# Performance work log

Hardware: AMD Instinct MI355X
Metric: run time of the kernel (lower is better)

## Reference

```python
import jax, jax.numpy as jnp
import numpy as np

CONF_THRES = 0.25
IOU_THRES = 0.45
MAX_DET = 1000
MAX_WH = 4096.0   # class offset for per-class NMS (yolov5 trick)
TOPK = 2048       # pre-NMS candidate cap (fixed-shape stand-in for max_nms)


def _xywh2xyxy(b):
    cx, cy, w, h = b[..., 0], b[..., 1], b[..., 2], b[..., 3]
    return jnp.stack([cx - w * 0.5, cy - h * 0.5, cx + w * 0.5, cy + h * 0.5], axis=-1)


def _box_iou(a, b):
    # a, b: [K, 4] in xyxy -> [K, K] pairwise IoU
    lt = jnp.maximum(a[:, None, :2], b[None, :, :2])
    rb = jnp.minimum(a[:, None, 2:], b[None, :, 2:])
    wh = jnp.clip(rb - lt, 0.0)
    inter = wh[..., 0] * wh[..., 1]
    area_a = (a[:, 2] - a[:, 0]) * (a[:, 3] - a[:, 1])
    area_b = (b[:, 2] - b[:, 0]) * (b[:, 3] - b[:, 1])
    return inter / (area_a[:, None] + area_b[None, :] - inter + 1e-7)


def _nms_single(pred):
    # pred: [N, 5+C] = (cx, cy, w, h, obj, cls...)
    obj = pred[:, 4]
    cls_prob = pred[:, 5:]
    cls_conf = jnp.max(cls_prob, axis=-1)
    cls_id = jnp.argmax(cls_prob, axis=-1)
    score = obj * cls_conf                      # conf = obj_conf * cls_conf (best class)
    valid = (obj > CONF_THRES) & (score > CONF_THRES)
    score = jnp.where(valid, score, 0.0)
    boxes = _xywh2xyxy(pred[:, :4])

    # keep top-K candidates by confidence (sorted descending)
    tops, idx = jax.lax.top_k(score, TOPK)
    boxes_k = boxes[idx]                        # [K, 4]
    cls_k = cls_id[idx]                         # [K]
    val_k = tops > 0.0

    # per-class NMS via class offset
    shifted = boxes_k + (cls_k.astype(boxes_k.dtype) * MAX_WH)[:, None]
    iou = _box_iou(shifted, shifted)            # [K, K]

    j = jnp.arange(TOPK)

    def body(i, keep):
        # if box i survives, suppress lower-scored boxes with IoU > thresh
        sup = keep[i] & (iou[i] > IOU_THRES) & (j > i)
        return keep & ~sup

    keep = jax.lax.fori_loop(0, TOPK, body, val_k)

    # gather up to MAX_DET kept detections (already score-sorted)
    fs, fi = jax.lax.top_k(jnp.where(keep, tops, -1.0), MAX_DET)
    ok = fs > 0.0
    det_boxes = jnp.where(ok[:, None], boxes_k[fi], 0.0)
    det_score = jnp.where(ok, tops[fi], 0.0)
    det_cls = jnp.where(ok, cls_k[fi].astype(det_boxes.dtype), -1.0)
    # [MAX_DET, 6] = (x1, y1, x2, y2, conf, cls); padded rows have conf 0, cls -1
    return jnp.concatenate([det_boxes, det_score[:, None], det_cls[:, None]], axis=-1)


def setup_inputs() -> dict:
    key = jax.random.key(0)
    raw = jax.random.uniform(key, (16, 25200, 85), dtype=jnp.float32)
    xy = raw[..., 0:2] * 640.0            # centers within a 640x640 image
    wh = raw[..., 2:4] * 120.0 + 2.0      # box sizes in [2, 122]
    rest = raw[..., 4:]                   # obj + class probs in [0, 1)
    pred = jnp.concatenate([xy, wh, rest], axis=-1)
    return {"pred": pred}


def reference(pred):
    return jax.vmap(_nms_single)(pred)
```

## Files before the change

kernel.cpp:

```cpp
#include <hip/hip_runtime.h>
#include <stdint.h>

#pragma clang fp contract(off)

#define BB 16
#define NN 25200
#define ROW 85
#define NCLS 80
#define TK 2048
#define SORTN 4096
#define NBIN 4096
#define MAXDET 1000
#define CONF 0.25f
#define IOUT 0.45f
#define SROWS 64
#define STH 0x3E800000u
#define MCAP 256

typedef float fvec4 __attribute__((ext_vector_type(4)));

#define AS1 __attribute__((address_space(1)))
#define AS3 __attribute__((address_space(3)))

__global__ __launch_bounds__(128) void score_kernel(const float* __restrict__ pred,
                                                    float* __restrict__ scores,
                                                    uint8_t* __restrict__ cls,
                                                    unsigned int* __restrict__ hist) {
  __shared__ __align__(16) float srow[SROWS * ROW];
  const int tile = blockIdx.x;
  const int b = blockIdx.y;
  const int tid = threadIdx.x;
  const int lane = tid & 63;
  const int row0 = tile * SROWS;
  int nrows = NN - row0;
  if (nrows > SROWS) nrows = SROWS;
  const char* gsrc = (const char*)(pred + ((size_t)b * NN + row0) * ROW);
  const int nbytes = nrows * ROW * 4;
  for (int off = tid * 16; off < nbytes; off += 128 * 16) {
    __builtin_amdgcn_global_load_lds((AS1 void*)(gsrc + off),
                                     (AS3 void*)((char*)srow + (off - lane * 16)),
                                     16, 0, 0);
  }
  __builtin_amdgcn_s_waitcnt(0);
  __syncthreads();
  if (tid < nrows) {
    const int n = row0 + tid;
    const float* r = srow + tid * ROW;
    float obj = r[4];
    float best = r[5];
    int bid = 0;
#pragma unroll
    for (int c = 1; c < NCLS; ++c) {
      float p = r[5 + c];
      if (p > best) { best = p; bid = c; }
    }
    float score = obj * best;
    bool valid = (obj > CONF) && (score > CONF);
    float sout = valid ? score : 0.0f;
    scores[(size_t)b * NN + n] = sout;
    cls[(size_t)b * NN + n] = (uint8_t)bid;
    if (valid) {
      unsigned int u = __float_as_uint(sout);
      unsigned int bin = (u - (STH + 1u)) >> 12;
      if (bin > NBIN - 1) bin = NBIN - 1;
      atomicAdd(&hist[(size_t)b * NBIN + bin], 1u);
    }
  }
}

__device__ __forceinline__ void suffix_scan_1024(const unsigned int* __restrict__ h,
                                                 unsigned int* soff, int* swsum,
                                                 int* sPP, int* sTT,
                                                 int t, int w, int lane) {
  int loc[4];
  int ssum = 0;
#pragma unroll
  for (int k = 0; k < 4; ++k) {
    loc[k] = (int)h[NBIN - 1 - (4 * t + k)];
    ssum += loc[k];
  }
  int v = ssum;
  for (int o = 1; o < 64; o <<= 1) { int uu = __shfl_up(v, o); if (lane >= o) v += uu; }
  if (lane == 63) swsum[w] = v;
  if (t == 0) *sPP = -1;
  __syncthreads();
  if (w == 0) {
    int x = (lane < 16) ? swsum[lane] : 0;
    for (int o = 1; o < 16; o <<= 1) { int uu = __shfl_up(x, o); if (lane >= o) x += uu; }
    if (lane < 16) swsum[lane] = x;
  }
  __syncthreads();
  const int total = swsum[15];
  int run = (w ? swsum[w - 1] : 0) + (v - ssum);
#pragma unroll
  for (int k = 0; k < 4; ++k) {
    int bin = NBIN - 1 - (4 * t + k);
    soff[bin] = (unsigned int)run;
    if (run < TK && run + loc[k] >= TK) { *sPP = bin; *sTT = run + loc[k]; }
    run += loc[k];
  }
  __syncthreads();
  if (t == 0 && *sPP < 0) { *sPP = 0; *sTT = total; }
  __syncthreads();
}

__global__ __launch_bounds__(1024) void scatter_kernel(const float* __restrict__ scores,
                                                       const unsigned int* __restrict__ hist,
                                                       unsigned int* __restrict__ gcnt,
                                                       unsigned long long* __restrict__ gskey) {
  const int b = blockIdx.y;
  const int t = threadIdx.x;
  const int w = t >> 6, lane = t & 63;
  __shared__ unsigned int soff[NBIN];
  __shared__ int swsum[16];
  __shared__ int sP, sT;
  suffix_scan_1024(hist + (size_t)b * NBIN, soff, swsum, &sP, &sT, t, w, lane);
  const int P = sP;
  const int n = blockIdx.x * 1024 + t;
  if (n >= NN) return;
  unsigned int u = __float_as_uint(scores[(size_t)b * NN + n]);
  if (u > STH) {
    unsigned int bin = (u - (STH + 1u)) >> 12;
    if (bin > NBIN - 1) bin = NBIN - 1;
    if ((int)bin >= P) {
      unsigned int pos = soff[bin] + atomicAdd(&gcnt[(size_t)b * NBIN + bin], 1u);
      if (pos < SORTN)
        gskey[(size_t)b * SORTN + pos] = ((unsigned long long)u << 32) | (unsigned int)(~n);
    }
  }
}

__global__ __launch_bounds__(1024) void emit_kernel(const float* __restrict__ pred,
                                                    const uint8_t* __restrict__ cls,
                                                    const unsigned int* __restrict__ hist,
                                                    const unsigned long long* __restrict__ gskey,
                                                    float* __restrict__ gtops,
                                                    fvec4* __restrict__ gbox,
                                                    int* __restrict__ gcls,
                                                    int* __restrict__ keep) {
  const int b = blockIdx.y;
  const int t = threadIdx.x;
  const int w = t >> 6, lane = t & 63;
  __shared__ unsigned int soff[NBIN];
  __shared__ int swsum[16];
  __shared__ int sP, sT;
  const unsigned int* h = hist + (size_t)b * NBIN;
  suffix_scan_1024(h, soff, swsum, &sP, &sT, t, w, lane);
  const int tot = sT;
  const int used = tot < SORTN ? tot : SORTN;
  const int npos = tot < TK ? tot : TK;
  const int pp = blockIdx.x * 1024 + t;
  int ip = npos + pp;
  if (ip < TK) {
    gtops[(size_t)b * TK + ip] = 0.0f;
    gcls[(size_t)b * TK + ip] = 0xFFFF;
    keep[(size_t)b * TK + ip] = 0;
    fvec4 z; z[0] = 0.f; z[1] = 0.f; z[2] = 0.f; z[3] = 0.f;
    gbox[(size_t)b * TK + ip] = z;
  }
  if (pp < used) {
    unsigned long long k = gskey[(size_t)b * SORTN + pp];
    unsigned int u = (unsigned int)(k >> 32);
    unsigned int bin = (u - (STH + 1u)) >> 12;
    if (bin > NBIN - 1) bin = NBIN - 1;
    int base = (int)soff[bin];
    int cnt = (int)h[bin];
    if (base + cnt > used) cnt = used - base;
    const unsigned long long* seg = gskey + (size_t)b * SORTN + base;
    int rank = 0;
    for (int j = 0; j < cnt; ++j) rank += (seg[j] > k) ? 1 : 0;
    int q = base + rank;
    if (q < npos) {
      int idx = (int)(~(unsigned int)k);
      gtops[(size_t)b * TK + q] = __uint_as_float(u);
      gcls[(size_t)b * TK + q] = (int)cls[(size_t)b * NN + idx];
      const float* rowp = pred + ((size_t)b * NN + idx) * ROW;
      float cx = rowp[0], cy = rowp[1], w2 = rowp[2], h2 = rowp[3];
      float hw = w2 * 0.5f, hh = h2 * 0.5f;
      fvec4 bb4;
      bb4[0] = cx - hw; bb4[1] = cy - hh; bb4[2] = cx + hw; bb4[3] = cy + hh;
      gbox[(size_t)b * TK + q] = bb4;
    }
  }
}

__global__ __launch_bounds__(64) void nms_kernel(const float* __restrict__ gtops,
                                                 const fvec4* __restrict__ gbox,
                                                 const int* __restrict__ gcls,
                                                 int* __restrict__ keep) {
  const int c = blockIdx.x;
  const int b = blockIdx.y;
  const int lane = threadIdx.x;
  __shared__ unsigned short spos[TK];
  __shared__ float mx1[MCAP], my1[MCAP], mx2[MCAP], my2[MCAP];
  __shared__ unsigned char skp[TK];

  int m = 0;
#pragma unroll 4
  for (int base = 0; base < TK; base += 64) {
    int j = base + lane;
    bool match = (gcls[(size_t)b * TK + j] == c);
    unsigned long long bal = __ballot(match);
    int mp = m + __popcll(bal & ((1ull << lane) - 1ull));
    if (match) {
      spos[mp] = (unsigned short)j;
      skp[mp] = (gtops[(size_t)b * TK + j] > 0.0f) ? 1 : 0;
      if (mp < MCAP) {
        fvec4 bx = gbox[(size_t)b * TK + j];
        mx1[mp] = bx[0]; my1[mp] = bx[1]; mx2[mp] = bx[2]; my2[mp] = bx[3];
      }
    }
    m += (int)__popcll(bal);
  }
  __syncthreads();

  float b0x1 = 0.f, b0y1 = 0.f, b0x2 = 0.f, b0y2 = 0.f;
  if (lane < m) { b0x1 = mx1[lane]; b0y1 = my1[lane]; b0x2 = mx2[lane]; b0y2 = my2[lane]; }
  __syncthreads();

  for (int i = 0; i < m; ++i) {
    if (!skp[i]) continue;
    float ax1, ay1, ax2, ay2;
    if (i < 64) {
      ax1 = __shfl(b0x1, i); ay1 = __shfl(b0y1, i);
      ax2 = __shfl(b0x2, i); ay2 = __shfl(b0y2, i);
    } else if (i < MCAP) {
      ax1 = mx1[i]; ay1 = my1[i]; ax2 = mx2[i]; ay2 = my2[i];
    } else {
      fvec4 bx = gbox[(size_t)b * TK + spos[i]];
      ax1 = bx[0]; ay1 = bx[1]; ax2 = bx[2]; ay2 = bx[3];
    }
    float aarea = (ax2 - ax1) * (ay2 - ay1);
    for (int q = 0; q * 64 < m; ++q) {
      int j = q * 64 + lane;
      if (j > i && j < m && skp[j]) {
        float jx1, jy1, jx2, jy2;
        if (q == 0) { jx1 = b0x1; jy1 = b0y1; jx2 = b0x2; jy2 = b0y2; }
        else if (j < MCAP) { jx1 = mx1[j]; jy1 = my1[j]; jx2 = mx2[j]; jy2 = my2[j]; }
        else { fvec4 bx = gbox[(size_t)b * TK + spos[j]];
               jx1 = bx[0]; jy1 = bx[1]; jx2 = bx[2]; jy2 = bx[3]; }
        float ltx = fmaxf(ax1, jx1), lty = fmaxf(ay1, jy1);
        float rbx = fminf(ax2, jx2), rby = fminf(ay2, jy2);
        float iw = fmaxf(rbx - ltx, 0.0f);
        float ih = fmaxf(rby - lty, 0.0f);
        float inter = iw * ih;
        float barea = (jx2 - jx1) * (jy2 - jy1);
        float iou = inter / (aarea + barea - inter + 1e-7f);
        if (iou > IOUT) skp[j] = 0;
      }
    }
  }
  __syncthreads();

  for (int i = lane; i < m; i += 64) {
    keep[(size_t)b * TK + spos[i]] = skp[i];
  }
}

__global__ __launch_bounds__(256) void out_kernel(const float* __restrict__ gtops,
                                                  const fvec4* __restrict__ gbox,
                                                  const int* __restrict__ gcls,
                                                  const int* __restrict__ keep,
                                                  float* __restrict__ out) {
  int b = blockIdx.x;
  int t = threadIdx.x;
  int w = t >> 6, lane = t & 63;
  __shared__ int sw4[4];
  const int CH = TK / 256;
  int base = t * CH;
  int kp[CH];
  int cnt = 0;
  for (int k = 0; k < CH; ++k) {
    kp[k] = keep[(size_t)b * TK + base + k];
    cnt += kp[k];
  }
  int v = cnt;
  for (int o = 1; o < 64; o <<= 1) { int u = __shfl_up(v, o); if (lane >= o) v += u; }
  if (lane == 63) sw4[w] = v;
  __syncthreads();
  int wbase = 0;
  for (int i = 0; i < w; ++i) wbase += sw4[i];
  int K = sw4[0] + sw4[1] + sw4[2] + sw4[3];
  int r = wbase + v - cnt;
  for (int k = 0; k < CH; ++k) {
    if (kp[k]) {
      if (r < MAXDET) {
        int j = base + k;
        float* o = out + ((size_t)b * MAXDET + r) * 6;
        fvec4 bx = gbox[(size_t)b * TK + j];
        o[0] = bx[0]; o[1] = bx[1]; o[2] = bx[2]; o[3] = bx[3];
        o[4] = gtops[(size_t)b * TK + j];
        o[5] = (float)gcls[(size_t)b * TK + j];
      }
      ++r;
    }
  }
  int Kc = K < MAXDET ? K : MAXDET;
  for (int r2 = Kc + t; r2 < MAXDET; r2 += 256) {
    float* o = out + ((size_t)b * MAXDET + r2) * 6;
    o[0] = 0.0f; o[1] = 0.0f; o[2] = 0.0f; o[3] = 0.0f; o[4] = 0.0f; o[5] = -1.0f;
  }
}

extern "C" void kernel_launch(void* const* d_in, const int* in_sizes, int n_in,
                              void* d_out, int out_size, void* d_ws, size_t ws_size,
                              hipStream_t stream) {
  const float* pred = (const float*)d_in[0];
  float* out = (float*)d_out;

  char* ws = (char*)d_ws;
  size_t off = 0;
  float*              scores = (float*)(ws + off);              off += (size_t)BB * NN * 4;
  uint8_t*            cls    = (uint8_t*)(ws + off);            off += (size_t)BB * NN;
  off = (off + 255) & ~(size_t)255;
  unsigned int*       hist   = (unsigned int*)(ws + off);       off += (size_t)BB * NBIN * 4;
  unsigned int*       gcnt   = (unsigned int*)(ws + off);       off += (size_t)BB * NBIN * 4;
  unsigned long long* gskey  = (unsigned long long*)(ws + off); off += (size_t)BB * SORTN * 8;
  float*              gtops  = (float*)(ws + off);              off += (size_t)BB * TK * 4;
  fvec4*              gbox   = (fvec4*)(ws + off);              off += (size_t)BB * TK * 16;
  int*                gcls   = (int*)(ws + off);                off += (size_t)BB * TK * 4;
  int*                keep   = (int*)(ws + off);                off += (size_t)BB * TK * 4;
  (void)ws_size; (void)in_sizes; (void)n_in; (void)out_size;

  hipMemsetAsync(hist, 0, (size_t)BB * NBIN * 4 * 2, stream);
  score_kernel<<<dim3((NN + SROWS - 1) / SROWS, BB), 128, 0, stream>>>(pred, scores, cls, hist);
  scatter_kernel<<<dim3((NN + 1023) / 1024, BB), 1024, 0, stream>>>(scores, hist, gcnt, gskey);
  emit_kernel<<<dim3(SORTN / 1024, BB), 1024, 0, stream>>>(pred, cls, hist, gskey,
                                                           gtops, gbox, gcls, keep);
  nms_kernel<<<dim3(NCLS, BB), 64, 0, stream>>>(gtops, gbox, gcls, keep);
  out_kernel<<<BB, 256, 0, stream>>>(gtops, gbox, gcls, keep, out);
}
```

Before: 244.4 us.

## Fuse scatter with emit and NMS with output via last-block-done counters

Merges the scatter and emit kernels, and the per-class NMS and output-compaction kernels, into two kernels. In each, the last block per batch to finish (found with an atomic done counter and thread fences) runs the follow-on stage. This removes two kernel launches and their inter-kernel gaps, and the done counters are cleared by the existing memset. The cost is that the emit and output stages now run in a single block per batch (1024 threads for emit, one 64-lane wave for output), which serializes work that was previously spread across blocks.

```diff
diff --git a/kernel.cpp b/kernel.cpp
--- a/kernel.cpp
+++ b/kernel.cpp
@@ -16,6 +16,7 @@
 #define SROWS 64
 #define STH 0x3E800000u
 #define MCAP 256
+#define SCB ((NN + 1023) / 1024)
 
 typedef float fvec4 __attribute__((ext_vector_type(4)));
 
@@ -104,61 +105,60 @@
   __syncthreads();
 }
 
-__global__ __launch_bounds__(1024) void scatter_kernel(const float* __restrict__ scores,
-                                                       const unsigned int* __restrict__ hist,
-                                                       unsigned int* __restrict__ gcnt,
-                                                       unsigned long long* __restrict__ gskey) {
+__global__ __launch_bounds__(1024) void scatter_emit_kernel(const float* __restrict__ pred,
+                                                            const uint8_t* __restrict__ cls,
+                                                            const float* __restrict__ scores,
+                                                            const unsigned int* __restrict__ hist,
+                                                            unsigned int* __restrict__ gcnt,
+                                                            unsigned int* __restrict__ done,
+                                                            unsigned long long* __restrict__ gskey,
+                                                            float* __restrict__ gtops,
+                                                            fvec4* __restrict__ gbox,
+                                                            int* __restrict__ gcls,
+                                                            int* __restrict__ keep) {
   const int b = blockIdx.y;
   const int t = threadIdx.x;
   const int w = t >> 6, lane = t & 63;
   __shared__ unsigned int soff[NBIN];
   __shared__ int swsum[16];
   __shared__ int sP, sT;
-  suffix_scan_1024(hist + (size_t)b * NBIN, soff, swsum, &sP, &sT, t, w, lane);
-  const int P = sP;
-  const int n = blockIdx.x * 1024 + t;
-  if (n >= NN) return;
-  unsigned int u = __float_as_uint(scores[(size_t)b * NN + n]);
-  if (u > STH) {
-    unsigned int bin = (u - (STH + 1u)) >> 12;
-    if (bin > NBIN - 1) bin = NBIN - 1;
-    if ((int)bin >= P) {
-      unsigned int pos = soff[bin] + atomicAdd(&gcnt[(size_t)b * NBIN + bin], 1u);
-      if (pos < SORTN)
-        gskey[(size_t)b * SORTN + pos] = ((unsigned long long)u << 32) | (unsigned int)(~n);
-    }
-  }
-}
-
-__global__ __launch_bounds__(1024) void emit_kernel(const float* __restrict__ pred,
-                                                    const uint8_t* __restrict__ cls,
-                                                    const unsigned int* __restrict__ hist,
-                                                    const unsigned long long* __restrict__ gskey,
-                                                    float* __restrict__ gtops,
-                                                    fvec4* __restrict__ gbox,
-                                                    int* __restrict__ gcls,
-                                                    int* __restrict__ keep) {
-  const int b = blockIdx.y;
-  const int t = threadIdx.x;
-  const int w = t >> 6, lane = t & 63;
-  __shared__ unsigned int soff[NBIN];
-  __shared__ int swsum[16];
-  __shared__ int sP, sT;
+  __shared__ int sLast;
   const unsigned int* h = hist + (size_t)b * NBIN;
   suffix_scan_1024(h, soff, swsum, &sP, &sT, t, w, lane);
+  const int P = sP;
+
+  const int n = blockIdx.x * 1024 + t;
+  if (n < NN) {
+    unsigned int u = __float_as_uint(scores[(size_t)b * NN + n]);
+    if (u > STH) {
+      unsigned int bin = (u - (STH + 1u)) >> 12;
+      if (bin > NBIN - 1) bin = NBIN - 1;
+      if ((int)bin >= P) {
+        unsigned int pos = soff[bin] + atomicAdd(&gcnt[(size_t)b * NBIN + bin], 1u);
+        if (pos < SORTN)
+          gskey[(size_t)b * SORTN + pos] = ((unsigned long long)u << 32) | (unsigned int)(~n);
+      }
+    }
+  }
+
+  __threadfence();
+  __syncthreads();
+  if (t == 0) sLast = (atomicAdd(&done[b], 1u) == SCB - 1) ? 1 : 0;
+  __syncthreads();
+  if (!sLast) return;
+  __threadfence();
+
   const int tot = sT;
   const int used = tot < SORTN ? tot : SORTN;
   const int npos = tot < TK ? tot : TK;
-  const int pp = blockIdx.x * 1024 + t;
-  int ip = npos + pp;
-  if (ip < TK) {
+  for (int ip = npos + t; ip < TK; ip += 1024) {
     gtops[(size_t)b * TK + ip] = 0.0f;
     gcls[(size_t)b * TK + ip] = 0xFFFF;
     keep[(size_t)b * TK + ip] = 0;
     fvec4 z; z[0] = 0.f; z[1] = 0.f; z[2] = 0.f; z[3] = 0.f;
     gbox[(size_t)b * TK + ip] = z;
   }
-  if (pp < used) {
+  for (int pp = t; pp < used; pp += 1024) {
     unsigned long long k = gskey[(size_t)b * SORTN + pp];
     unsigned int u = (unsigned int)(k >> 32);
     unsigned int bin = (u - (STH + 1u)) >> 12;
@@ -184,16 +184,19 @@
   }
 }
 
-__global__ __launch_bounds__(64) void nms_kernel(const float* __restrict__ gtops,
-                                                 const fvec4* __restrict__ gbox,
-                                                 const int* __restrict__ gcls,
-                                                 int* __restrict__ keep) {
+__global__ __launch_bounds__(64) void nms_out_kernel(const float* __restrict__ gtops,
+                                                     const fvec4* __restrict__ gbox,
+                                                     const int* __restrict__ gcls,
+                                                     unsigned int* __restrict__ done2,
+                                                     int* __restrict__ keep,
+                                                     float* __restrict__ out) {
   const int c = blockIdx.x;
   const int b = blockIdx.y;
   const int lane = threadIdx.x;
   __shared__ unsigned short spos[TK];
   __shared__ float mx1[MCAP], my1[MCAP], mx2[MCAP], my2[MCAP];
   __shared__ unsigned char skp[TK];
+  __shared__ int sLast;
 
   int m = 0;
 #pragma unroll 4
@@ -255,37 +258,32 @@
   for (int i = lane; i < m; i += 64) {
     keep[(size_t)b * TK + spos[i]] = skp[i];
   }
-}
-
-__global__ __launch_bounds__(256) void out_kernel(const float* __restrict__ gtops,
-                                                  const fvec4* __restrict__ gbox,
-                                                  const int* __restrict__ gcls,
-                                                  const int* __restrict__ keep,
-                                                  float* __restrict__ out) {
-  int b = blockIdx.x;
-  int t = threadIdx.x;
-  int w = t >> 6, lane = t & 63;
-  __shared__ int sw4[4];
-  const int CH = TK / 256;
-  int base = t * CH;
+
+  __threadfence();
+  __syncthreads();
+  if (lane == 0) sLast = (atomicAdd(&done2[b], 1u) == NCLS - 1) ? 1 : 0;
+  __syncthreads();
+  if (!sLast) return;
+  __threadfence();
+
+  const int CH = TK / 64;
+  int base2 = lane * CH;
   int kp[CH];
   int cnt = 0;
+#pragma unroll
   for (int k = 0; k < CH; ++k) {
-    kp[k] = keep[(size_t)b * TK + base + k];
+    kp[k] = keep[(size_t)b * TK + base2 + k];
     cnt += kp[k];
   }
   int v = cnt;
   for (int o = 1; o < 64; o <<= 1) { int u = __shfl_up(v, o); if (lane >= o) v += u; }
-  if (lane == 63) sw4[w] = v;
-  __syncthreads();
-  int wbase = 0;
-  for (int i = 0; i < w; ++i) wbase += sw4[i];
-  int K = sw4[0] + sw4[1] + sw4[2] + sw4[3];
-  int r = wbase + v - cnt;
+  int K = __shfl(v, 63);
+  int r = v - cnt;
+#pragma unroll
   for (int k = 0; k < CH; ++k) {
     if (kp[k]) {
       if (r < MAXDET) {
-        int j = base + k;
+        int j = base2 + k;
         float* o = out + ((size_t)b * MAXDET + r) * 6;
         fvec4 bx = gbox[(size_t)b * TK + j];
         o[0] = bx[0]; o[1] = bx[1]; o[2] = bx[2]; o[3] = bx[3];
@@ -296,7 +294,7 @@
     }
   }
   int Kc = K < MAXDET ? K : MAXDET;
-  for (int r2 = Kc + t; r2 < MAXDET; r2 += 256) {
+  for (int r2 = Kc + lane; r2 < MAXDET; r2 += 64) {
     float* o = out + ((size_t)b * MAXDET + r2) * 6;
     o[0] = 0.0f; o[1] = 0.0f; o[2] = 0.0f; o[3] = 0.0f; o[4] = 0.0f; o[5] = -1.0f;
   }
@@ -315,6 +313,9 @@
   off = (off + 255) & ~(size_t)255;
   unsigned int*       hist   = (unsigned int*)(ws + off);       off += (size_t)BB * NBIN * 4;
   unsigned int*       gcnt   = (unsigned int*)(ws + off);       off += (size_t)BB * NBIN * 4;
+  unsigned int*       done   = (unsigned int*)(ws + off);       off += (size_t)BB * 4;
+  unsigned int*       done2  = (unsigned int*)(ws + off);       off += (size_t)BB * 4;
+  const size_t zbytes = (size_t)BB * NBIN * 4 * 2 + (size_t)BB * 4 * 2;
   unsigned long long* gskey  = (unsigned long long*)(ws + off); off += (size_t)BB * SORTN * 8;
   float*              gtops  = (float*)(ws + off);              off += (size_t)BB * TK * 4;
   fvec4*              gbox   = (fvec4*)(ws + off);              off += (size_t)BB * TK * 16;
@@ -322,11 +323,9 @@
   int*                keep   = (int*)(ws + off);                off += (size_t)BB * TK * 4;
   (void)ws_size; (void)in_sizes; (void)n_in; (void)out_size;
 
-  hipMemsetAsync(hist, 0, (size_t)BB * NBIN * 4 * 2, stream);
+  hipMemsetAsync(hist, 0, zbytes, stream);
   score_kernel<<<dim3((NN + SROWS - 1) / SROWS, BB), 128, 0, stream>>>(pred, scores, cls, hist);
-  scatter_kernel<<<dim3((NN + 1023) / 1024, BB), 1024, 0, stream>>>(scores, hist, gcnt, gskey);
-  emit_kernel<<<dim3(SORTN / 1024, BB), 1024, 0, stream>>>(pred, cls, hist, gskey,
-                                                           gtops, gbox, gcls, keep);
-  nms_kernel<<<dim3(NCLS, BB), 64, 0, stream>>>(gtops, gbox, gcls, keep);
-  out_kernel<<<BB, 256, 0, stream>>>(gtops, gbox, gcls, keep, out);
-}
+  scatter_emit_kernel<<<dim3(SCB, BB), 1024, 0, stream>>>(pred, cls, scores, hist, gcnt, done,
+                                                          gskey, gtops, gbox, gcls, keep);
+  nms_out_kernel<<<dim3(NCLS, BB), 64, 0, stream>>>(gtops, gbox, gcls, done2, keep, out);
+}
```

Result: slower. 444.7 us (+82.0%).
